# Performance work log

Hardware: AMD Instinct MI355X
Metric: run time of the kernel (lower is better)

## Reference

```python
import jax, jax.numpy as jnp
import numpy as np

N_NODES = 100000
N_EDGES = 1600000
IN_DIM, HID_DIM, OUT_DIM = 512, 128, 64
BN_EPS = 1e-5


def setup_inputs() -> dict:
    key = jax.random.key(0)
    ks = jax.random.split(key, 8)
    x = jax.random.normal(ks[0], (N_NODES, IN_DIM), dtype=jnp.float32)
    edge_index = jax.random.randint(ks[1], (2, N_EDGES), 0, N_NODES, dtype=jnp.int64)
    W1 = jax.random.normal(ks[2], (IN_DIM, HID_DIM), dtype=jnp.float32) / np.sqrt(IN_DIM)
    b1 = jnp.zeros((HID_DIM,), dtype=jnp.float32)
    W2 = jax.random.normal(ks[3], (HID_DIM, OUT_DIM), dtype=jnp.float32) / np.sqrt(HID_DIM)
    b2 = jnp.zeros((OUT_DIM,), dtype=jnp.float32)
    gamma = jnp.ones((HID_DIM,), dtype=jnp.float32)
    beta = jnp.zeros((HID_DIM,), dtype=jnp.float32)
    return {"x": x, "edge_index": edge_index, "W1": W1, "b1": b1,
            "W2": W2, "b2": b2, "gamma": gamma, "beta": beta}


def _gcn_conv(x, src, dst, W, b):
    # PyG GCNConv(normalize=False): transform then sum-aggregate src->dst, no self-loops
    h = x @ W                                   # [N, out]
    agg = jax.ops.segment_sum(h[src], dst, num_segments=N_NODES)
    return agg + b


def _batchnorm(h, gamma, beta):
    mean = jnp.mean(h, axis=0)
    var = jnp.mean(jnp.square(h - mean), axis=0)  # biased var (training mode)
    return (h - mean) * jax.lax.rsqrt(var + BN_EPS) * gamma + beta


def reference(x, edge_index, W1, b1, W2, b2, gamma, beta):
    src, dst = edge_index[0], edge_index[1]
    h = _gcn_conv(x, src, dst, W1, b1)          # [N, HID]
    h = _batchnorm(h, gamma, beta)
    h = jax.nn.relu(h)
    h = _gcn_conv(h, src, dst, W2, b2)          # [N, OUT]
    # F.normalize(p=2, dim=1), eps=1e-12
    norm = jnp.linalg.norm(h, axis=1, keepdims=True)
    return h / jnp.maximum(norm, 1e-12)
```

## Files before the change

kernel.cpp:

```cpp
#include <hip/hip_runtime.h>
#include <hip/hip_bf16.h>
#include <stdint.h>

#define NN 100000
#define NE 1600000
#define IND 512
#define HID 128
#define OUTD 64
#define BN_EPS 1e-5f
#define NP 98
#define PSZ 1024
#define PCAP 20480
#define BINCH 8192
#define NBIN 196

typedef __attribute__((ext_vector_type(8))) short short8v;
typedef __attribute__((ext_vector_type(4))) float f32x4;

__device__ __forceinline__ ushort f2bf(float f, float& back) {
  uint u = __float_as_uint(f);
  uint r = u + 0x7FFFu + ((u >> 16) & 1u);
  ushort h = (ushort)(r >> 16);
  back = __uint_as_float(((uint)h) << 16);
  return h;
}
__device__ __forceinline__ ushort f2bf_n(float f) {
  uint u = __float_as_uint(f);
  uint r = u + 0x7FFFu + ((u >> 16) & 1u);
  return (ushort)(r >> 16);
}
__device__ __forceinline__ float bf2f(ushort h) {
  return __uint_as_float(((uint)h) << 16);
}
__device__ __forceinline__ float bflo(uint v) { return __uint_as_float(v << 16); }
__device__ __forceinline__ float bfhi(uint v) { return __uint_as_float(v & 0xffff0000u); }
__device__ __forceinline__ uint packbf(float lo, float hi) {
  return (uint)f2bf_n(lo) | ((uint)f2bf_n(hi) << 16);
}

__device__ __forceinline__ int edge_at(const int* e32, int f, int i) {
  if (f) return (int)((const long long*)e32)[i];
  return e32[i];
}

__global__ __launch_bounds__(256) void k_prep(const int* __restrict__ edges,
                                              const float* __restrict__ W1,
                                              const float* __restrict__ W2,
                                              int* __restrict__ flag,
                                              ushort* __restrict__ Wth,
                                              ushort* __restrict__ Wtl,
                                              ushort* __restrict__ W2th,
                                              ushort* __restrict__ W2tl) {
  const int bid = blockIdx.x, tid = threadIdx.x;
  if (bid == 0) {
    __shared__ int nz;
    if (tid == 0) nz = 0;
    __syncthreads();
    if (tid < 64) {
      int v = edges[2 * tid + 1];
      if (v != 0) atomicAdd(&nz, 1);
    }
    __syncthreads();
    if (tid == 0) *flag = (nz == 0) ? 1 : 0;
    return;
  }
  if (bid <= 256) {
    int i = (bid - 1) * 256 + tid;
    int n = i >> 9, k = i & 511;
    float w = W1[(size_t)k * HID + n];
    float back;
    Wth[i] = f2bf(w, back);
    Wtl[i] = f2bf_n(w - back);
    return;
  }
  {
    int j = (bid - 257) * 256 + tid;
    int n = j >> 7, k = j & 127;
    float w = W2[(size_t)k * OUTD + n];
    float back;
    W2th[j] = f2bf(w, back);
    W2tl[j] = f2bf_n(w - back);
  }
}

__device__ void bin_body(int bid, ushort* smem16, const int* edges,
                         const int* flag, int* gCursor, int* staging) {
  int* cnt   = (int*)smem16;
  int* scn   = cnt + 128;
  int* base  = cnt + 256;
  int* cur   = cnt + 384;
  int* items = cnt + 512;
  const int tid = threadIdx.x;
  const int e0 = bid * BINCH;
  const int ecnt = min(BINCH, NE - e0);
  const int f = *flag;
  for (int i = tid; i < NP; i += 256) cnt[i] = 0;
  __syncthreads();
  for (int i = tid; i < ecnt; i += 256) {
    int d = edge_at(edges, f, NE + e0 + i);
    atomicAdd(&cnt[d >> 10], 1);
  }
  __syncthreads();
  if (tid == 0) {
    int s = 0;
    for (int p = 0; p < NP; ++p) { scn[p] = s; s += cnt[p]; }
  }
  __syncthreads();
  if (tid < NP) {
    base[tid] = (cnt[tid] > 0) ? atomicAdd(&gCursor[tid], cnt[tid]) : 0;
    cur[tid] = 0;
  }
  __syncthreads();
  for (int i = tid; i < ecnt; i += 256) {
    int d = edge_at(edges, f, NE + e0 + i);
    int s = edge_at(edges, f, e0 + i);
    int p = d >> 10;
    int lp = atomicAdd(&cur[p], 1);
    items[scn[p] + lp] = (s << 10) | (d & (PSZ - 1));
  }
  __syncthreads();
  for (int p = 0; p < NP; ++p) {
    int c = cnt[p];
    if (c == 0) continue;
    int gb = base[p];
    int* dst = staging + (size_t)p * PCAP;
    for (int i = tid; i < c; i += 256) {
      int gpos = gb + i;
      if (gpos < PCAP) dst[gpos] = items[scn[p] + i];
    }
  }
}

__device__ __forceinline__ void g1_loadA(const float* x, int row0, int tid,
                                         int kt, float4 ra[4]) {
#pragma unroll
  for (int i = 0; i < 4; ++i) {
    int flat = i * 256 + tid, r = flat >> 3, kq = flat & 7;
    int grow = row0 + r; if (grow > NN - 1) grow = NN - 1;
    ra[i] = *(const float4*)(x + (size_t)grow * IND + kt + kq * 4);
  }
}
__device__ __forceinline__ void g1_loadB(const ushort* Wth, const ushort* Wtl,
                                         int tid, int kt, uint4 rbh[2], uint4 rbl[2]) {
#pragma unroll
  for (int i = 0; i < 2; ++i) {
    int flat = i * 256 + tid, col = flat >> 2, kc = flat & 3;
    rbh[i] = *(const uint4*)(Wth + (size_t)col * IND + kt + kc * 8);
    rbl[i] = *(const uint4*)(Wtl + (size_t)col * IND + kt + kc * 8);
  }
}
__device__ __forceinline__ void g1_storeA(ushort* dAh, int tid, const float4 ra[4]) {
#pragma unroll
  for (int i = 0; i < 4; ++i) {
    int flat = i * 256 + tid, r = flat >> 3, kq = flat & 7;
    ushort4 hi;
    hi.x = f2bf_n(ra[i].x); hi.y = f2bf_n(ra[i].y);
    hi.z = f2bf_n(ra[i].z); hi.w = f2bf_n(ra[i].w);
    *(ushort4*)&dAh[r * 40 + kq * 4] = hi;
  }
}
__device__ __forceinline__ void g1_storeB(ushort* dBh, ushort* dBl, int tid,
                                          const uint4 rbh[2], const uint4 rbl[2]) {
#pragma unroll
  for (int i = 0; i < 2; ++i) {
    int flat = i * 256 + tid, col = flat >> 2, kc = flat & 3;
    *(uint4*)&dBh[col * 40 + kc * 8] = rbh[i];
    *(uint4*)&dBl[col * 40 + kc * 8] = rbl[i];
  }
}
__device__ __forceinline__ void g1_mfma(const ushort* buf, int wr, int wc,
                                        int lrow, int lkg, f32x4 acc[4][4]) {
  const ushort* bAh = buf;
  const ushort* bBh = buf + 5120;
  const ushort* bBl = buf + 10240;
  short8v ah[4], bh[4], bl[4];
#pragma unroll
  for (int m = 0; m < 4; ++m) {
    int r = wr * 64 + m * 16 + lrow;
    ah[m] = *(const short8v*)&bAh[r * 40 + lkg * 8];
  }
#pragma unroll
  for (int n = 0; n < 4; ++n) {
    int c = wc * 64 + n * 16 + lrow;
    bh[n] = *(const short8v*)&bBh[c * 40 + lkg * 8];
    bl[n] = *(const short8v*)&bBl[c * 40 + lkg * 8];
  }
#pragma unroll
  for (int m = 0; m < 4; ++m)
#pragma unroll
    for (int n = 0; n < 4; ++n) {
      acc[m][n] = __builtin_amdgcn_mfma_f32_16x16x32_bf16(ah[m], bh[n], acc[m][n], 0, 0, 0);
      acc[m][n] = __builtin_amdgcn_mfma_f32_16x16x32_bf16(ah[m], bl[n], acc[m][n], 0, 0, 0);
    }
}
__device__ __forceinline__ void g1_barrier() {
  asm volatile("s_waitcnt lgkmcnt(0)");
  __builtin_amdgcn_sched_barrier(0);
  __builtin_amdgcn_s_barrier();
  __builtin_amdgcn_sched_barrier(0);
}

__device__ void gemm1_body(int bid, ushort* smem, const float* x,
                           const ushort* Wth, const ushort* Wtl,
                           ushort* h1b) {
  ushort* sOut = smem;
  const int tid = threadIdx.x;
  const int lane = tid & 63, wid = tid >> 6;
  const int wr = wid >> 1, wc = wid & 1;
  const int lrow = lane & 15, lkg = lane >> 4;
  const int row0 = bid * 128;
  ushort* B0 = smem;
  ushort* B1 = smem + 15360;

  f32x4 acc[4][4];
#pragma unroll
  for (int m = 0; m < 4; ++m)
#pragma unroll
    for (int n = 0; n < 4; ++n) acc[m][n] = (f32x4){0.f, 0.f, 0.f, 0.f};

  float4 raA0[4], raA1[4];
  uint4 rbh[2], rbl[2];

  g1_loadA(x, row0, tid, 0, raA0);
  g1_loadA(x, row0, tid, 32, raA1);
  g1_loadB(Wth, Wtl, tid, 0, rbh, rbl);
  g1_storeA(B0, tid, raA0);
  g1_storeB(B0 + 5120, B0 + 10240, tid, rbh, rbl);
  g1_barrier();

  for (int ss = 0; ss < 8; ++ss) {
    int s0 = 2 * ss;
    if (s0 + 2 < 16) g1_loadA(x, row0, tid, (s0 + 2) * 32, raA0);
    g1_loadB(Wth, Wtl, tid, (s0 + 1) * 32, rbh, rbl);
    g1_mfma(B0, wr, wc, lrow, lkg, acc);
    g1_storeA(B1, tid, raA1);
    g1_storeB(B1 + 5120, B1 + 10240, tid, rbh, rbl);
    g1_barrier();

    int s1 = s0 + 1;
    if (s1 + 2 < 16) {
      g1_loadA(x, row0, tid, (s1 + 2) * 32, raA1);
    }
    if (s1 + 1 < 16) {
      g1_loadB(Wth, Wtl, tid, (s1 + 1) * 32, rbh, rbl);
    }
    g1_mfma(B1, wr, wc, lrow, lkg, acc);
    if (s1 + 1 < 16) {
      g1_storeA(B0, tid, raA0);
      g1_storeB(B0 + 5120, B0 + 10240, tid, rbh, rbl);
      g1_barrier();
    }
  }

  __syncthreads();
#pragma unroll
  for (int m = 0; m < 4; ++m)
#pragma unroll
    for (int i = 0; i < 4; ++i) {
      int lr = wr * 64 + m * 16 + lkg * 4 + i;
#pragma unroll
      for (int n = 0; n < 4; ++n)
        sOut[lr * 136 + wc * 64 + n * 16 + lrow] = f2bf_n(acc[m][n][i]);
    }
  __syncthreads();
#pragma unroll
  for (int j = 0; j < 8; ++j) {
    int flat = j * 256 + tid;
    int r = flat >> 4, c = flat & 15;
    int grow = row0 + r;
    if (grow < NN)
      *(uint4*)(h1b + (size_t)grow * HID + c * 8) =
          *(const uint4*)&sOut[r * 136 + c * 8];
  }
}

__global__ __launch_bounds__(256) void k_fused1(const float* __restrict__ x,
                                                const ushort* __restrict__ Wth,
                                                const ushort* __restrict__ Wtl,
                                                const int* __restrict__ edges,
                                                const int* __restrict__ flag,
                                                int* __restrict__ gCursor,
                                                int* __restrict__ staging,
                                                ushort* __restrict__ h1b) {
  __shared__ __align__(16) ushort smem[30720];
  if (blockIdx.x < NBIN)
    bin_body(blockIdx.x, smem, edges, flag, gCursor, staging);
  else
    gemm1_body(blockIdx.x - NBIN, smem, x, Wth, Wtl, h1b);
}

__global__ __launch_bounds__(256) void k_csrpart(const int* __restrict__ staging,
                                                 const int* __restrict__ gCursor,
                                                 int* __restrict__ offsets,
                                                 int* __restrict__ csr_src) {
  __shared__ int cnt[PSZ];
  __shared__ int cur[PSZ];
  __shared__ int tsum[256];
  __shared__ int gc[256];
  __shared__ int srcbuf[PCAP];
  const int tid = threadIdx.x;
  const int p = blockIdx.x;
  gc[tid] = (tid < NP) ? min(gCursor[tid], PCAP) : 0;
  for (int i = tid; i < PSZ; i += 256) { cnt[i] = 0; cur[i] = 0; }
  if (p == NP - 1 && tid == 0) offsets[NN] = NE;
  __syncthreads();
  for (int off = 1; off < 128; off <<= 1) {
    int t = (tid >= off) ? gc[tid - off] : 0;
    __syncthreads();
    gc[tid] += t;
    __syncthreads();
  }
  const int tot = min(gCursor[p], PCAP);
  const int gbase = gc[p] - tot;
  const int* st = staging + (size_t)p * PCAP;
  for (int i = tid; i < tot; i += 256) atomicAdd(&cnt[st[i] & (PSZ - 1)], 1);
  __syncthreads();
  int b0 = tid * 4;
  int c0 = cnt[b0], c1 = cnt[b0 + 1], c2 = cnt[b0 + 2], c3 = cnt[b0 + 3];
  int ls = c0 + c1 + c2 + c3;
  tsum[tid] = ls;
  __syncthreads();
  for (int off = 1; off < 256; off <<= 1) {
    int t = (tid >= off) ? tsum[tid - off] : 0;
    __syncthreads();
    tsum[tid] += t;
    __syncthreads();
  }
  int ebase = tsum[tid] - ls;
  cnt[b0] = ebase;
  cnt[b0 + 1] = ebase + c0;
  cnt[b0 + 2] = ebase + c0 + c1;
  cnt[b0 + 3] = ebase + c0 + c1 + c2;
  __syncthreads();
  for (int i = tid; i < PSZ; i += 256) {
    int node = p * PSZ + i;
    if (node < NN) offsets[node] = gbase + cnt[i];
  }
  for (int i = tid; i < tot; i += 256) {
    int item = st[i];
    int dl = item & (PSZ - 1);
    int lp = atomicAdd(&cur[dl], 1);
    srcbuf[cnt[dl] + lp] = item >> 10;
  }
  __syncthreads();
  for (int i = tid; i < tot; i += 256) csr_src[gbase + i] = srcbuf[i];
}

__global__ __launch_bounds__(256) void k_agg1(const ushort* __restrict__ h1b,
                                              const int* __restrict__ offsets,
                                              const int* __restrict__ csr_src,
                                              const float* __restrict__ b1,
                                              ushort* __restrict__ aggb) {
  int w = threadIdx.x >> 6, lane = threadIdx.x & 63;
  int n = blockIdx.x * 4 + w;
  if (n >= NN) return;
  int beg = offsets[n], end = offsets[n + 1];
  int q4 = lane >> 4, ch = lane & 15;
  const uint4* h = (const uint4*)h1b;
  float4 aL = {0.f, 0.f, 0.f, 0.f}, aH = {0.f, 0.f, 0.f, 0.f};
  float4 cL = {0.f, 0.f, 0.f, 0.f}, cH = {0.f, 0.f, 0.f, 0.f};
  int i = beg + q4;
  for (; i + 4 < end; i += 8) {
    uint4 v0 = h[(size_t)csr_src[i] * 16 + ch];
    uint4 v1 = h[(size_t)csr_src[i + 4] * 16 + ch];
    aL.x += bflo(v0.x); aL.y += bfhi(v0.x); aL.z += bflo(v0.y); aL.w += bfhi(v0.y);
    aH.x += bflo(v0.z); aH.y += bfhi(v0.z); aH.z += bflo(v0.w); aH.w += bfhi(v0.w);
    cL.x += bflo(v1.x); cL.y += bfhi(v1.x); cL.z += bflo(v1.y); cL.w += bfhi(v1.y);
    cH.x += bflo(v1.z); cH.y += bfhi(v1.z); cH.z += bflo(v1.w); cH.w += bfhi(v1.w);
  }
  for (; i < end; i += 4) {
    uint4 v = h[(size_t)csr_src[i] * 16 + ch];
    aL.x += bflo(v.x); aL.y += bfhi(v.x); aL.z += bflo(v.y); aL.w += bfhi(v.y);
    aH.x += bflo(v.z); aH.y += bfhi(v.z); aH.z += bflo(v.w); aH.w += bfhi(v.w);
  }
  aL.x += cL.x; aL.y += cL.y; aL.z += cL.z; aL.w += cL.w;
  aH.x += cH.x; aH.y += cH.y; aH.z += cH.z; aH.w += cH.w;
  aL.x += __shfl_xor(aL.x, 16); aL.x += __shfl_xor(aL.x, 32);
  aL.y += __shfl_xor(aL.y, 16); aL.y += __shfl_xor(aL.y, 32);
  aL.z += __shfl_xor(aL.z, 16); aL.z += __shfl_xor(aL.z, 32);
  aL.w += __shfl_xor(aL.w, 16); aL.w += __shfl_xor(aL.w, 32);
  aH.x += __shfl_xor(aH.x, 16); aH.x += __shfl_xor(aH.x, 32);
  aH.y += __shfl_xor(aH.y, 16); aH.y += __shfl_xor(aH.y, 32);
  aH.z += __shfl_xor(aH.z, 16); aH.z += __shfl_xor(aH.z, 32);
  aH.w += __shfl_xor(aH.w, 16); aH.w += __shfl_xor(aH.w, 32);
  if (q4 == 0) {
    float4 bLo = *(const float4*)(b1 + 8 * ch);
    float4 bHi = *(const float4*)(b1 + 8 * ch + 4);
    uint4 o;
    o.x = packbf(aL.x + bLo.x, aL.y + bLo.y);
    o.y = packbf(aL.z + bLo.z, aL.w + bLo.w);
    o.z = packbf(aH.x + bHi.x, aH.y + bHi.y);
    o.w = packbf(aH.z + bHi.z, aH.w + bHi.w);
    ((uint4*)aggb)[(size_t)n * 16 + ch] = o;
  }
}

__global__ __launch_bounds__(256) void k_bnstats(const ushort* __restrict__ aggb,
                                                 float* __restrict__ gsum,
                                                 float* __restrict__ gsq) {
  __shared__ float2 ss[4][64], qq[4][64];
  int tid = threadIdx.x;
  int lane = tid & 63, g = tid >> 6;
  int r0 = blockIdx.x * 128;
  const uint* a = (const uint*)aggb;
  float2 s = {0.f, 0.f}, q = {0.f, 0.f};
  for (int k = 0; k < 32; ++k) {
    int r = r0 + g + 4 * k;
    if (r < NN) {
      uint v = a[(size_t)r * 64 + lane];
      float lo = bflo(v), hi = bfhi(v);
      s.x += lo; s.y += hi;
      q.x += lo * lo; q.y += hi * hi;
    }
  }
  ss[g][lane] = s; qq[g][lane] = q;
  __syncthreads();
  if (g == 0) {
    float2 S = ss[0][lane], Q = qq[0][lane];
#pragma unroll
    for (int gg = 1; gg < 4; ++gg) {
      S.x += ss[gg][lane].x; S.y += ss[gg][lane].y;
      Q.x += qq[gg][lane].x; Q.y += qq[gg][lane].y;
    }
    atomicAdd(&gsum[2 * lane], S.x);
    atomicAdd(&gsum[2 * lane + 1], S.y);
    atomicAdd(&gsq[2 * lane], Q.x);
    atomicAdd(&gsq[2 * lane + 1], Q.y);
  }
}

__global__ __launch_bounds__(256) void k_gemm2m(const ushort* __restrict__ aggb,
                                                const ushort* __restrict__ W2th,
                                                const ushort* __restrict__ W2tl,
                                                const float* __restrict__ gsum,
                                                const float* __restrict__ gsq,
                                                const float* __restrict__ gamma,
                                                const float* __restrict__ beta,
                                                ushort* __restrict__ h2b) {
  __shared__ __align__(16) ushort smem[27648];
  __shared__ float isgS[128], bbS[128];
  ushort* sBh = smem;
  ushort* sBl = smem + 8704;
  ushort* sA  = smem + 17408;
  ushort* sOut = sA;
  const int tid = threadIdx.x;
  const int lane = tid & 63, wid = tid >> 6;
  const int wr = wid >> 1, wc = wid & 1;
  const int lrow = lane & 15, lkg = lane >> 4;
  const int row0 = blockIdx.x * 128;

  if (tid < 128) {
    float mean = gsum[tid] * (1.f / NN);
    float var = fmaxf(gsq[tid] * (1.f / NN) - mean * mean, 0.f);
    float inv = 1.f / sqrtf(var + BN_EPS);
    float g = gamma[tid] * inv;
    isgS[tid] = g;
    bbS[tid] = beta[tid] - mean * g;
  }
#pragma unroll
  for (int i = 0; i < 4; ++i) {
    int c = i * 256 + tid;
    int n = c >> 4, kq = c & 15;
    *(uint4*)&sBh[n * 136 + kq * 8] = *(const uint4*)(W2th + (size_t)n * HID + kq * 8);
    *(uint4*)&sBl[n * 136 + kq * 8] = *(const uint4*)(W2tl + (size_t)n * HID + kq * 8);
  }

  f32x4 acc[4][2];
#pragma unroll
  for (int m = 0; m < 4; ++m)
#pragma unroll
    for (int n = 0; n < 2; ++n) acc[m][n] = (f32x4){0.f, 0.f, 0.f, 0.f};

  uint4 rA[2];
#pragma unroll
  for (int i = 0; i < 2; ++i) {
    int c = i * 256 + tid;
    int r = c >> 2, cq = c & 3;
    int grow = row0 + r; if (grow > NN - 1) grow = NN - 1;
    rA[i] = *(const uint4*)(aggb + (size_t)grow * HID + cq * 8);
  }
  __syncthreads();

  {
    ushort* dA = sA;
#pragma unroll
    for (int i = 0; i < 2; ++i) {
      int c = i * 256 + tid;
      int r = c >> 2, cq = c & 3;
      int k0 = cq * 8;
      uint4 v = rA[i];
      uint o[4];
      const uint* vv = (const uint*)&v;
#pragma unroll
      for (int j = 0; j < 4; ++j) {
        float lo = bflo(vv[j]), hi = bfhi(vv[j]);
        lo = fmaxf(fmaf(lo, isgS[k0 + 2 * j], bbS[k0 + 2 * j]), 0.f);
        hi = fmaxf(fmaf(hi, isgS[k0 + 2 * j + 1], bbS[k0 + 2 * j + 1]), 0.f);
        o[j] = packbf(lo, hi);
      }
      *(uint4*)&dA[r * 40 + cq * 8] = *(const uint4*)o;
    }
  }

  int cur = 0;
  for (int s = 0; s < 4; ++s) {
    __syncthreads();
    const int kt = s * 32;
    if (s < 3) {
      int ktn = kt + 32;
#pragma unroll
      for (int i = 0; i < 2; ++i) {
        int c = i * 256 + tid;
        int r = c >> 2, cq = c & 3;
        int grow = row0 + r; if (grow > NN - 1) grow = NN - 1;
        rA[i] = *(const uint4*)(aggb + (size_t)grow * HID + ktn + cq * 8);
      }
    }
    {
      const ushort* bA = sA + cur * 5120;
      short8v ah[4], bh[2], bl[2];
#pragma unroll
      for (int m = 0; m < 4; ++m) {
        int r = wr * 64 + m * 16 + lrow;
        ah[m] = *(const short8v*)&bA[r * 40 + lkg * 8];
      }
#pragma unroll
      for (int n = 0; n < 2; ++n) {
        int c = wc * 32 + n * 16 + lrow;
        bh[n] = *(const short8v*)&sBh[c * 136 + kt + lkg * 8];
        bl[n] = *(const short8v*)&sBl[c * 136 + kt + lkg * 8];
      }
#pragma unroll
      for (int m = 0; m < 4; ++m)
#pragma unroll
        for (int n = 0; n < 2; ++n) {
          acc[m][n] = __builtin_amdgcn_mfma_f32_16x16x32_bf16(ah[m], bh[n], acc[m][n], 0, 0, 0);
          acc[m][n] = __builtin_amdgcn_mfma_f32_16x16x32_bf16(ah[m], bl[n], acc[m][n], 0, 0, 0);
        }
    }
    if (s < 3) {
      ushort* dA = sA + (cur ^ 1) * 5120;
      int k0b = (s + 1) * 32;
#pragma unroll
      for (int i = 0; i < 2; ++i) {
        int c = i * 256 + tid;
        int r = c >> 2, cq = c & 3;
        int k0 = k0b + cq * 8;
        uint4 v = rA[i];
        uint o[4];
        const uint* vv = (const uint*)&v;
#pragma unroll
        for (int j = 0; j < 4; ++j) {
          float lo = bflo(vv[j]), hi = bfhi(vv[j]);
          lo = fmaxf(fmaf(lo, isgS[k0 + 2 * j], bbS[k0 + 2 * j]), 0.f);
          hi = fmaxf(fmaf(hi, isgS[k0 + 2 * j + 1], bbS[k0 + 2 * j + 1]), 0.f);
          o[j] = packbf(lo, hi);
        }
        *(uint4*)&dA[r * 40 + cq * 8] = *(const uint4*)o;
      }
    }
    cur ^= 1;
  }

  __syncthreads();
#pragma unroll
  for (int m = 0; m < 4; ++m)
#pragma unroll
    for (int i = 0; i < 4; ++i) {
      int lr = wr * 64 + m * 16 + lkg * 4 + i;
#pragma unroll
      for (int n = 0; n < 2; ++n)
        sOut[lr * 72 + wc * 32 + n * 16 + lrow] = f2bf_n(acc[m][n][i]);
    }
  __syncthreads();
#pragma unroll
  for (int i = 0; i < 4; ++i) {
    int c = i * 256 + tid;
    int r = c >> 3, cq = c & 7;
    int grow = row0 + r;
    if (grow < NN)
      *(uint4*)(h2b + (size_t)grow * OUTD + cq * 8) =
          *(const uint4*)&sOut[r * 72 + cq * 8];
  }
}

__global__ __launch_bounds__(256) void k_agg2norm(const ushort* __restrict__ h2b,
                                                  const int* __restrict__ offsets,
                                                  const int* __restrict__ csr_src,
                                                  const float* __restrict__ b2,
                                                  float* __restrict__ out) {
  int w = threadIdx.x >> 6, lane = threadIdx.x & 63;
  int n = blockIdx.x * 4 + w;
  if (n >= NN) return;
  int beg = offsets[n], end = offsets[n + 1];
  int q4 = lane >> 4, ch = lane & 15;
  const uint2* h = (const uint2*)h2b;
  float4 a = {0.f, 0.f, 0.f, 0.f}, c4 = {0.f, 0.f, 0.f, 0.f};
  int i = beg + q4;
  for (; i + 4 < end; i += 8) {
    uint2 v0 = h[(size_t)csr_src[i] * 16 + ch];
    uint2 v1 = h[(size_t)csr_src[i + 4] * 16 + ch];
    a.x += bflo(v0.x); a.y += bfhi(v0.x); a.z += bflo(v0.y); a.w += bfhi(v0.y);
    c4.x += bflo(v1.x); c4.y += bfhi(v1.x); c4.z += bflo(v1.y); c4.w += bfhi(v1.y);
  }
  for (; i < end; i += 4) {
    uint2 v = h[(size_t)csr_src[i] * 16 + ch];
    a.x += bflo(v.x); a.y += bfhi(v.x); a.z += bflo(v.y); a.w += bfhi(v.y);
  }
  a.x += c4.x; a.y += c4.y; a.z += c4.z; a.w += c4.w;
  a.x += __shfl_xor(a.x, 16); a.x += __shfl_xor(a.x, 32);
  a.y += __shfl_xor(a.y, 16); a.y += __shfl_xor(a.y, 32);
  a.z += __shfl_xor(a.z, 16); a.z += __shfl_xor(a.z, 32);
  a.w += __shfl_xor(a.w, 16); a.w += __shfl_xor(a.w, 32);
  float4 b = *(const float4*)(b2 + 4 * ch);
  a.x += b.x; a.y += b.y; a.z += b.z; a.w += b.w;
  float q = a.x * a.x + a.y * a.y + a.z * a.z + a.w * a.w;
#pragma unroll
  for (int off = 8; off > 0; off >>= 1) q += __shfl_xor(q, off);
  float norm = sqrtf(q);
  float scale = 1.f / fmaxf(norm, 1e-12f);
  if (q4 == 0) {
    float4 o = {a.x * scale, a.y * scale, a.z * scale, a.w * scale};
    *(float4*)(out + (size_t)n * OUTD + 4 * ch) = o;
  }
}

extern "C" void kernel_launch(void* const* d_in, const int* in_sizes, int n_in,
                              void* d_out, int out_size, void* d_ws, size_t ws_size,
                              hipStream_t stream) {
  const float* x     = (const float*)d_in[0];
  const int*   edges = (const int*)d_in[1];
  const float* W1    = (const float*)d_in[2];
  const float* b1    = (const float*)d_in[3];
  const float* W2    = (const float*)d_in[4];
  const float* b2    = (const float*)d_in[5];
  const float* gamma = (const float*)d_in[6];
  const float* beta  = (const float*)d_in[7];

  char* ws = (char*)d_ws;
  ushort* h1b     = (ushort*)(ws);
  ushort* aggb    = (ushort*)(ws + 26000000);
  int*    csr_src = (int*)(ws + 77500000);
  int*    offsets = (int*)(ws + 84000000);
  int*    staging = (int*)(ws + 84400128);
  int*    gCursor = (int*)(ws + 92428544);
  float*  gsum    = (float*)(ws + 92429568);
  float*  gsq     = (float*)(ws + 92430080);
  int*    eflag   = (int*)(ws + 92431616);
  ushort* Wth     = (ushort*)(ws + 92432128);
  ushort* Wtl     = (ushort*)(ws + 92563200);
  ushort* W2th    = (ushort*)(ws + 92694272);
  ushort* W2tl    = (ushort*)(ws + 92710656);
  ushort* h2b     = h1b;

  if (ws_size < 92727040) return;

  hipMemsetAsync(gCursor, 0, 2048, stream);

  k_prep<<<289, 256, 0, stream>>>(edges, W1, W2, eflag, Wth, Wtl, W2th, W2tl);
  k_fused1<<<NBIN + 782, 256, 0, stream>>>(x, Wth, Wtl, edges, eflag,
                                           gCursor, staging, h1b);
  k_csrpart<<<NP, 256, 0, stream>>>(staging, gCursor, offsets, csr_src);
  k_agg1<<<25000, 256, 0, stream>>>(h1b, offsets, csr_src, b1, aggb);
  k_bnstats<<<782, 256, 0, stream>>>(aggb, gsum, gsq);
  k_gemm2m<<<782, 256, 0, stream>>>(aggb, W2th, W2tl, gsum, gsq, gamma, beta, h2b);
  k_agg2norm<<<25000, 256, 0, stream>>>(h2b, offsets, csr_src, b2,
                                        (float*)d_out);
}
```

Measured before the change: 282.5 us.

## Load GEMM1 weight fragments straight into registers and deepen gather unrolling

The first GEMM no longer stages the split-bf16 W1 tiles through shared memory. Each wave loads its B fragments directly from global memory into registers, double-buffered two k-steps ahead, and only the A tile goes through LDS. This cuts the LDS footprint from 30720 to 17408 ushorts, which can raise occupancy of the fused kernel, and drops the B store/load traffic. Both neighbor-aggregation kernels now unroll the edge gather to four independent loads with four accumulators, to keep more memory requests in flight. The trade-offs are higher register pressure and redundant global loads of W across waves.

```diff
diff --git a/kernel.cpp b/kernel.cpp
--- a/kernel.cpp
+++ b/kernel.cpp
@@ -36,6 +36,13 @@
 __device__ __forceinline__ float bfhi(uint v) { return __uint_as_float(v & 0xffff0000u); }
 __device__ __forceinline__ uint packbf(float lo, float hi) {
   return (uint)f2bf_n(lo) | ((uint)f2bf_n(hi) << 16);
+}
+__device__ __forceinline__ void acc8(float4& L, float4& H, uint4 v) {
+  L.x += bflo(v.x); L.y += bfhi(v.x); L.z += bflo(v.y); L.w += bfhi(v.y);
+  H.x += bflo(v.z); H.y += bfhi(v.z); H.z += bflo(v.w); H.w += bfhi(v.w);
+}
+__device__ __forceinline__ void acc4(float4& L, uint2 v) {
+  L.x += bflo(v.x); L.y += bfhi(v.x); L.z += bflo(v.y); L.w += bfhi(v.y);
 }
 
 __device__ __forceinline__ int edge_at(const int* e32, int f, int i) {
@@ -140,15 +147,6 @@
     ra[i] = *(const float4*)(x + (size_t)grow * IND + kt + kq * 4);
   }
 }
-__device__ __forceinline__ void g1_loadB(const ushort* Wth, const ushort* Wtl,
-                                         int tid, int kt, uint4 rbh[2], uint4 rbl[2]) {
-#pragma unroll
-  for (int i = 0; i < 2; ++i) {
-    int flat = i * 256 + tid, col = flat >> 2, kc = flat & 3;
-    rbh[i] = *(const uint4*)(Wth + (size_t)col * IND + kt + kc * 8);
-    rbl[i] = *(const uint4*)(Wtl + (size_t)col * IND + kt + kc * 8);
-  }
-}
 __device__ __forceinline__ void g1_storeA(ushort* dAh, int tid, const float4 ra[4]) {
 #pragma unroll
   for (int i = 0; i < 4; ++i) {
@@ -159,31 +157,24 @@
     *(ushort4*)&dAh[r * 40 + kq * 4] = hi;
   }
 }
-__device__ __forceinline__ void g1_storeB(ushort* dBh, ushort* dBl, int tid,
-                                          const uint4 rbh[2], const uint4 rbl[2]) {
-#pragma unroll
-  for (int i = 0; i < 2; ++i) {
-    int flat = i * 256 + tid, col = flat >> 2, kc = flat & 3;
-    *(uint4*)&dBh[col * 40 + kc * 8] = rbh[i];
-    *(uint4*)&dBl[col * 40 + kc * 8] = rbl[i];
-  }
-}
-__device__ __forceinline__ void g1_mfma(const ushort* buf, int wr, int wc,
-                                        int lrow, int lkg, f32x4 acc[4][4]) {
-  const ushort* bAh = buf;
-  const ushort* bBh = buf + 5120;
-  const ushort* bBl = buf + 10240;
-  short8v ah[4], bh[4], bl[4];
+__device__ __forceinline__ void g1_loadBfrag(const ushort* Wth, const ushort* Wtl,
+                                             int wc, int lrow, int lkg, int kt,
+                                             short8v bh[4], short8v bl[4]) {
+#pragma unroll
+  for (int n = 0; n < 4; ++n) {
+    int c = wc * 64 + n * 16 + lrow;
+    bh[n] = *(const short8v*)(Wth + (size_t)c * IND + kt + lkg * 8);
+    bl[n] = *(const short8v*)(Wtl + (size_t)c * IND + kt + lkg * 8);
+  }
+}
+__device__ __forceinline__ void g1_mfmaR(const ushort* bAh, const short8v bh[4],
+                                         const short8v bl[4], int wr,
+                                         int lrow, int lkg, f32x4 acc[4][4]) {
+  short8v ah[4];
 #pragma unroll
   for (int m = 0; m < 4; ++m) {
     int r = wr * 64 + m * 16 + lrow;
     ah[m] = *(const short8v*)&bAh[r * 40 + lkg * 8];
-  }
-#pragma unroll
-  for (int n = 0; n < 4; ++n) {
-    int c = wc * 64 + n * 16 + lrow;
-    bh[n] = *(const short8v*)&bBh[c * 40 + lkg * 8];
-    bl[n] = *(const short8v*)&bBl[c * 40 + lkg * 8];
   }
 #pragma unroll
   for (int m = 0; m < 4; ++m)
@@ -203,14 +194,14 @@
 __device__ void gemm1_body(int bid, ushort* smem, const float* x,
                            const ushort* Wth, const ushort* Wtl,
                            ushort* h1b) {
+  ushort* A0 = smem;
+  ushort* A1 = smem + 5120;
   ushort* sOut = smem;
   const int tid = threadIdx.x;
   const int lane = tid & 63, wid = tid >> 6;
   const int wr = wid >> 1, wc = wid & 1;
   const int lrow = lane & 15, lkg = lane >> 4;
   const int row0 = bid * 128;
-  ushort* B0 = smem;
-  ushort* B1 = smem + 15360;
 
   f32x4 acc[4][4];
 #pragma unroll
@@ -219,35 +210,29 @@
     for (int n = 0; n < 4; ++n) acc[m][n] = (f32x4){0.f, 0.f, 0.f, 0.f};
 
   float4 raA0[4], raA1[4];
-  uint4 rbh[2], rbl[2];
+  short8v bhA[4], blA[4], bhB[4], blB[4];
 
   g1_loadA(x, row0, tid, 0, raA0);
   g1_loadA(x, row0, tid, 32, raA1);
-  g1_loadB(Wth, Wtl, tid, 0, rbh, rbl);
-  g1_storeA(B0, tid, raA0);
-  g1_storeB(B0 + 5120, B0 + 10240, tid, rbh, rbl);
+  g1_loadBfrag(Wth, Wtl, wc, lrow, lkg, 0, bhA, blA);
+  g1_loadBfrag(Wth, Wtl, wc, lrow, lkg, 32, bhB, blB);
+  g1_storeA(A0, tid, raA0);
   g1_barrier();
 
   for (int ss = 0; ss < 8; ++ss) {
-    int s0 = 2 * ss;
+    const int s0 = 2 * ss;
     if (s0 + 2 < 16) g1_loadA(x, row0, tid, (s0 + 2) * 32, raA0);
-    g1_loadB(Wth, Wtl, tid, (s0 + 1) * 32, rbh, rbl);
-    g1_mfma(B0, wr, wc, lrow, lkg, acc);
-    g1_storeA(B1, tid, raA1);
-    g1_storeB(B1 + 5120, B1 + 10240, tid, rbh, rbl);
+    g1_mfmaR(A0, bhA, blA, wr, lrow, lkg, acc);
+    if (s0 + 2 < 16) g1_loadBfrag(Wth, Wtl, wc, lrow, lkg, (s0 + 2) * 32, bhA, blA);
+    g1_storeA(A1, tid, raA1);
     g1_barrier();
 
-    int s1 = s0 + 1;
-    if (s1 + 2 < 16) {
-      g1_loadA(x, row0, tid, (s1 + 2) * 32, raA1);
-    }
+    const int s1 = s0 + 1;
+    if (s1 + 2 < 16) g1_loadA(x, row0, tid, (s1 + 2) * 32, raA1);
+    g1_mfmaR(A1, bhB, blB, wr, lrow, lkg, acc);
+    if (s1 + 2 < 16) g1_loadBfrag(Wth, Wtl, wc, lrow, lkg, (s1 + 2) * 32, bhB, blB);
     if (s1 + 1 < 16) {
-      g1_loadB(Wth, Wtl, tid, (s1 + 1) * 32, rbh, rbl);
-    }
-    g1_mfma(B1, wr, wc, lrow, lkg, acc);
-    if (s1 + 1 < 16) {
-      g1_storeA(B0, tid, raA0);
-      g1_storeB(B0 + 5120, B0 + 10240, tid, rbh, rbl);
+      g1_storeA(A0, tid, raA0);
       g1_barrier();
     }
   }
@@ -282,7 +267,7 @@
                                                 int* __restrict__ gCursor,
                                                 int* __restrict__ staging,
                                                 ushort* __restrict__ h1b) {
-  __shared__ __align__(16) ushort smem[30720];
+  __shared__ __align__(16) ushort smem[17408];
   if (blockIdx.x < NBIN)
     bin_body(blockIdx.x, smem, edges, flag, gCursor, staging);
   else
@@ -357,24 +342,31 @@
   int beg = offsets[n], end = offsets[n + 1];
   int q4 = lane >> 4, ch = lane & 15;
   const uint4* h = (const uint4*)h1b;
-  float4 aL = {0.f, 0.f, 0.f, 0.f}, aH = {0.f, 0.f, 0.f, 0.f};
-  float4 cL = {0.f, 0.f, 0.f, 0.f}, cH = {0.f, 0.f, 0.f, 0.f};
+  float4 aL = {0.f,0.f,0.f,0.f}, aH = {0.f,0.f,0.f,0.f};
+  float4 bL = {0.f,0.f,0.f,0.f}, bH = {0.f,0.f,0.f,0.f};
+  float4 cL = {0.f,0.f,0.f,0.f}, cH = {0.f,0.f,0.f,0.f};
+  float4 dL = {0.f,0.f,0.f,0.f}, dH = {0.f,0.f,0.f,0.f};
   int i = beg + q4;
+  for (; i + 12 < end; i += 16) {
+    uint4 v0 = h[(size_t)csr_src[i] * 16 + ch];
+    uint4 v1 = h[(size_t)csr_src[i + 4] * 16 + ch];
+    uint4 v2 = h[(size_t)csr_src[i + 8] * 16 + ch];
+    uint4 v3 = h[(size_t)csr_src[i + 12] * 16 + ch];
+    acc8(aL, aH, v0); acc8(bL, bH, v1); acc8(cL, cH, v2); acc8(dL, dH, v3);
+  }
   for (; i + 4 < end; i += 8) {
     uint4 v0 = h[(size_t)csr_src[i] * 16 + ch];
     uint4 v1 = h[(size_t)csr_src[i + 4] * 16 + ch];
-    aL.x += bflo(v0.x); aL.y += bfhi(v0.x); aL.z += bflo(v0.y); aL.w += bfhi(v0.y);
-    aH.x += bflo(v0.z); aH.y += bfhi(v0.z); aH.z += bflo(v0.w); aH.w += bfhi(v0.w);
-    cL.x += bflo(v1.x); cL.y += bfhi(v1.x); cL.z += bflo(v1.y); cL.w += bfhi(v1.y);
-    cH.x += bflo(v1.z); cH.y += bfhi(v1.z); cH.z += bflo(v1.w); cH.w += bfhi(v1.w);
+    acc8(aL, aH, v0); acc8(bL, bH, v1);
   }
   for (; i < end; i += 4) {
     uint4 v = h[(size_t)csr_src[i] * 16 + ch];
-    aL.x += bflo(v.x); aL.y += bfhi(v.x); aL.z += bflo(v.y); aL.w += bfhi(v.y);
-    aH.x += bflo(v.z); aH.y += bfhi(v.z); aH.z += bflo(v.w); aH.w += bfhi(v.w);
-  }
-  aL.x += cL.x; aL.y += cL.y; aL.z += cL.z; aL.w += cL.w;
-  aH.x += cH.x; aH.y += cH.y; aH.z += cH.z; aH.w += cH.w;
+    acc8(aL, aH, v);
+  }
+  aL.x += bL.x + cL.x + dL.x; aL.y += bL.y + cL.y + dL.y;
+  aL.z += bL.z + cL.z + dL.z; aL.w += bL.w + cL.w + dL.w;
+  aH.x += bH.x + cH.x + dH.x; aH.y += bH.y + cH.y + dH.y;
+  aH.z += bH.z + cH.z + dH.z; aH.w += bH.w + cH.w + dH.w;
   aL.x += __shfl_xor(aL.x, 16); aL.x += __shfl_xor(aL.x, 32);
   aL.y += __shfl_xor(aL.y, 16); aL.y += __shfl_xor(aL.y, 32);
   aL.z += __shfl_xor(aL.z, 16); aL.z += __shfl_xor(aL.z, 32);
@@ -595,19 +587,27 @@
   int beg = offsets[n], end = offsets[n + 1];
   int q4 = lane >> 4, ch = lane & 15;
   const uint2* h = (const uint2*)h2b;
-  float4 a = {0.f, 0.f, 0.f, 0.f}, c4 = {0.f, 0.f, 0.f, 0.f};
+  float4 a = {0.f,0.f,0.f,0.f}, b4 = {0.f,0.f,0.f,0.f};
+  float4 c4 = {0.f,0.f,0.f,0.f}, d4 = {0.f,0.f,0.f,0.f};
   int i = beg + q4;
+  for (; i + 12 < end; i += 16) {
+    uint2 v0 = h[(size_t)csr_src[i] * 16 + ch];
+    uint2 v1 = h[(size_t)csr_src[i + 4] * 16 + ch];
+    uint2 v2 = h[(size_t)csr_src[i + 8] * 16 + ch];
+    uint2 v3 = h[(size_t)csr_src[i + 12] * 16 + ch];
+    acc4(a, v0); acc4(b4, v1); acc4(c4, v2); acc4(d4, v3);
+  }
   for (; i + 4 < end; i += 8) {
     uint2 v0 = h[(size_t)csr_src[i] * 16 + ch];
     uint2 v1 = h[(size_t)csr_src[i + 4] * 16 + ch];
-    a.x += bflo(v0.x); a.y += bfhi(v0.x); a.z += bflo(v0.y); a.w += bfhi(v0.y);
-    c4.x += bflo(v1.x); c4.y += bfhi(v1.x); c4.z += bflo(v1.y); c4.w += bfhi(v1.y);
+    acc4(a, v0); acc4(b4, v1);
   }
   for (; i < end; i += 4) {
     uint2 v = h[(size_t)csr_src[i] * 16 + ch];
-    a.x += bflo(v.x); a.y += bfhi(v.x); a.z += bflo(v.y); a.w += bfhi(v.y);
-  }
-  a.x += c4.x; a.y += c4.y; a.z += c4.z; a.w += c4.w;
+    acc4(a, v);
+  }
+  a.x += b4.x + c4.x + d4.x; a.y += b4.y + c4.y + d4.y;
+  a.z += b4.z + c4.z + d4.z; a.w += b4.w + c4.w + d4.w;
   a.x += __shfl_xor(a.x, 16); a.x += __shfl_xor(a.x, 32);
   a.y += __shfl_xor(a.y, 16); a.y += __shfl_xor(a.y, 32);
   a.z += __shfl_xor(a.z, 16); a.z += __shfl_xor(a.z, 32);
```

Result: slower. 308.2 us (+9.1%).
